# Kernel optimization log

Measured on AMD Instinct MI355X. Metric: run time of the kernel, lower is better.

The kernel has to match this reference:

```python
import jax, jax.numpy as jnp
import numpy as np

N, VQ, VK, C, H = 4, 4096, 4096, 128, 64


def setup_inputs() -> dict:
    key = jax.random.key(0)
    kx, ky, kq, kk, kv = jax.random.split(key, 5)
    # xavier-uniform-ish scale for params
    def xavier(k, shape):
        fan_in, fan_out = shape
        lim = (6.0 / (fan_in + fan_out)) ** 0.5
        return jax.random.uniform(k, shape, jnp.float32, -lim, lim)
    return {
        "x": jax.random.normal(kx, (N, VQ, C), jnp.float32),
        "y": jax.random.normal(ky, (N, VK, C), jnp.float32),
        "Wq": xavier(kq, (C, H)),
        "Wk": xavier(kk, (C, H)),
        "Wv": xavier(kv, (C, C)),
    }


def reference(x, y, Wq, Wk, Wv):
    # x: [n, vq, c], y: [n, vk, c]
    scale = Wq.shape[1] ** (-0.5)
    q = jnp.einsum('nvc,co->nvo', x, Wq)   # [n, vq, h]
    k = jnp.einsum('nvc,co->nvo', y, Wk)   # [n, vk, h]
    v = jnp.einsum('nvc,co->nvo', y, Wv)   # [n, vk, c]
    scores = jnp.einsum('nqc,nkc->nqk', q, k) * scale  # [n, vq, vk]
    attn = jax.nn.softmax(scores, axis=-1)
    return jnp.einsum('nqk,nkc->nqc', attn, v)         # [n, vq, c]
```

## Files before the change

kernel.cpp:

```cpp
#include <hip/hip_runtime.h>

typedef __bf16 bf16x8 __attribute__((ext_vector_type(8)));
typedef __bf16 bf16x4 __attribute__((ext_vector_type(4)));
typedef __bf16 bf16x2 __attribute__((ext_vector_type(2)));
typedef float  f32x4  __attribute__((ext_vector_type(4)));
typedef float  f32x16 __attribute__((ext_vector_type(16)));
typedef int    i32x4  __attribute__((ext_vector_type(4)));

#define MFMA16 __builtin_amdgcn_mfma_f32_16x16x32_bf16
#define MFMA32 __builtin_amdgcn_mfma_f32_32x32x16_bf16

static constexpr int BATCH = 4;
static constexpr int SEQ   = 4096;
static constexpr int CDIM  = 128;
static constexpr int HDIM  = 64;
static constexpr float FIXMAX = 16.0f;

union FB2  { bf16x2 h; int i; };
union I4B8 { i32x4 i; bf16x8 b; };

__device__ inline bf16x8 load8f_cvt(const float* __restrict__ p) {
    f32x4 a = *reinterpret_cast<const f32x4*>(p);
    f32x4 b = *reinterpret_cast<const f32x4*>(p + 4);
    bf16x8 r;
    r[0] = (__bf16)a[0]; r[1] = (__bf16)a[1]; r[2] = (__bf16)a[2]; r[3] = (__bf16)a[3];
    r[4] = (__bf16)b[0]; r[5] = (__bf16)b[1]; r[6] = (__bf16)b[2]; r[7] = (__bf16)b[3];
    return r;
}


__global__ __launch_bounds__(256) void proj_all_kernel(
    const float* __restrict__ x, const float* __restrict__ y,
    const float* __restrict__ Wq, const float* __restrict__ Wk,
    const float* __restrict__ Wv,
    __bf16* __restrict__ Qw, __bf16* __restrict__ Kw, __bf16* __restrict__ Vtw,
    float qscale)
{
    __shared__ __bf16 Wt[64][136];
    __shared__ __bf16 Vtile[64][72];

    const int job = blockIdx.x >> 8;
    const int bx  = blockIdx.x & 255;
    const int t    = threadIdx.x;
    const int lane = t & 63;
    const int w    = t >> 6;
    const int m    = lane & 15;
    const int quad = lane >> 4;

    if (job <= 1) {
        const float* X    = job ? y  : x;
        const float* W    = job ? Wk : Wq;
        __bf16*      outp = job ? Kw : Qw;
        const float scale = job ? 1.0f : qscale;

        #pragma unroll
        for (int pass = 0; pass < 4; ++pass) {
            int flat = pass * 2048 + t * 8;
            int cin  = flat >> 6;
            int h0   = flat & 63;
            bf16x8 v = load8f_cvt(W + flat);
            #pragma unroll
            for (int j = 0; j < 8; ++j) Wt[h0 + j][cin] = v[j];
        }
        __syncthreads();

        const int row0 = bx * 64 + w * 16;
        bf16x8 af[4];
        #pragma unroll
        for (int kc = 0; kc < 4; ++kc)
            af[kc] = load8f_cvt(X + (long)(row0 + m) * 128 + kc * 32 + quad * 8);

        #pragma unroll
        for (int tn = 0; tn < 4; ++tn) {
            f32x4 acc = {0.f, 0.f, 0.f, 0.f};
            #pragma unroll
            for (int kc = 0; kc < 4; ++kc) {
                bf16x8 bfrag = *reinterpret_cast<const bf16x8*>(&Wt[tn * 16 + m][kc * 32 + quad * 8]);
                acc = MFMA16(af[kc], bfrag, acc, 0, 0, 0);
            }
            #pragma unroll
            for (int r = 0; r < 4; ++r) {
                int  kg   = row0 + quad * 4 + r;
                long addr = ((long)(kg >> 5) * 4 + tn) * 512
                          + ((m >> 3) * 32 + (kg & 31)) * 8 + (m & 7);
                outp[addr] = (__bf16)(acc[r] * scale);
            }
        }
    } else {
        const int cob = (job - 2) * 64;
        const int ct0 = (job - 2) * 2;

        #pragma unroll
        for (int pass = 0; pass < 4; ++pass) {
            int flat = pass * 2048 + t * 8;
            int cin  = flat >> 6;
            int co0  = flat & 63;
            bf16x8 v = load8f_cvt(Wv + cin * 128 + cob + co0);
            #pragma unroll
            for (int j = 0; j < 8; ++j) Wt[co0 + j][cin] = v[j];
        }
        __syncthreads();

        const int row0 = bx * 64 + w * 16;
        bf16x8 af[4];
        #pragma unroll
        for (int kc = 0; kc < 4; ++kc)
            af[kc] = load8f_cvt(y + (long)(row0 + m) * 128 + kc * 32 + quad * 8);

        #pragma unroll
        for (int tn = 0; tn < 4; ++tn) {
            f32x4 acc = {0.f, 0.f, 0.f, 0.f};
            #pragma unroll
            for (int kc = 0; kc < 4; ++kc) {
                bf16x8 bfrag = *reinterpret_cast<const bf16x8*>(&Wt[tn * 16 + m][kc * 32 + quad * 8]);
                acc = MFMA16(af[kc], bfrag, acc, 0, 0, 0);
            }
            bf16x4 pk;
            #pragma unroll
            for (int r = 0; r < 4; ++r) pk[r] = (__bf16)acc[r];
            *reinterpret_cast<bf16x4*>(&Vtile[tn * 16 + m][w * 16 + quad * 4]) = pk;
        }
        __syncthreads();

        #pragma unroll
        for (int pp = 0; pp < 2; ++pp) {
            int i       = pp * 256 + t;
            int c_local = i & 31;
            int hh      = (i >> 5) & 1;
            int kc2     = (i >> 6) & 1;
            int ct_l    = (i >> 7) & 1;
            int kt_l    = i >> 8;
            bf16x8 v = *reinterpret_cast<const bf16x8*>(
                &Vtile[ct_l * 32 + c_local][kt_l * 32 + kc2 * 16 + hh * 8]);
            long dst = ((long)(bx * 2 + kt_l) * 8 + (ct0 + ct_l) * 2 + kc2) * 512
                     + (hh * 32 + c_local) * 8;
            *reinterpret_cast<bf16x8*>(Vtw + dst) = v;
        }
    }
}

__device__ __forceinline__ void attn_step(
    const bf16x8 (&kf)[4], const bf16x8 (&vf)[8], const bf16x8 (&qf)[4],
    f32x16 (&o_acc)[4], float& l_a, float& l_b, int h)
{
    f32x16 s;
    #pragma unroll
    for (int i = 0; i < 16; ++i) s[i] = -FIXMAX;
    #pragma unroll
    for (int kc = 0; kc < 4; ++kc)
        s = MFMA32(kf[kc], qf[kc], s, 0, 0, 0);

    int Dw[8];
    #pragma unroll
    for (int r2 = 0; r2 < 8; ++r2) {
        float p0 = __builtin_amdgcn_exp2f(s[2 * r2]);
        float p1 = __builtin_amdgcn_exp2f(s[2 * r2 + 1]);
        l_a += p0; l_b += p1;
        FB2 u; u.h[0] = (__bf16)p0; u.h[1] = (__bf16)p1;
        Dw[r2] = u.i;
    }

    #pragma unroll
    for (int kc2 = 0; kc2 < 2; ++kc2) {
        int a0 = Dw[4 * kc2 + 0], a1 = Dw[4 * kc2 + 1];
        int a2 = Dw[4 * kc2 + 2], a3 = Dw[4 * kc2 + 3];
        int r0 = __shfl_xor(a0, 32, 64);
        int r1 = __shfl_xor(a1, 32, 64);
        int r2 = __shfl_xor(a2, 32, 64);
        int r3 = __shfl_xor(a3, 32, 64);
        I4B8 pb;
        pb.i[0] = h ? r2 : a0;
        pb.i[1] = h ? r3 : a1;
        pb.i[2] = h ? a2 : r0;
        pb.i[3] = h ? a3 : r1;
        #pragma unroll
        for (int ct = 0; ct < 4; ++ct)
            o_acc[ct] = MFMA32(vf[ct * 2 + kc2], pb.b, o_acc[ct], 0, 0, 0);
    }
}

__global__ __launch_bounds__(512, 2) void attn_kernel(
    const __bf16* __restrict__ Qs, const __bf16* __restrict__ Ks,
    const __bf16* __restrict__ Vs, float* __restrict__ out)
{
    __shared__ float mg[2][64][68];

    const int t    = threadIdx.x;
    const int lane = t & 63;
    const int w    = t >> 6;
    const int qh   = w & 1;
    const int g    = w >> 1;
    const int qc   = lane & 31;
    const int h    = lane >> 5;

    const int bx = blockIdx.x;
    const int n  = (bx >> 1) & 3;
    const int qt = (bx >> 3) * 2 + (bx & 1);
    const int q0 = qt * 64 + qh * 32;

    const long QT = (long)n * 128 + (q0 >> 5);
    bf16x8 qf[4];
    #pragma unroll
    for (int kc = 0; kc < 4; ++kc)
        qf[kc] = *reinterpret_cast<const bf16x8*>(Qs + (QT * 4 + kc) * 512 + lane * 8);

    const __bf16* kb = Ks + ((long)n * 128 + g * 32) * 2048 + lane * 8;
    const __bf16* vb = Vs + ((long)n * 128 + g * 32) * 4096 + lane * 8;

    f32x16 o_acc[4];
    #pragma unroll
    for (int ct = 0; ct < 4; ++ct)
        #pragma unroll
        for (int i = 0; i < 16; ++i) o_acc[ct][i] = 0.f;
    float l_a = 0.f, l_b = 0.f;

    bf16x8 kfA[4], vfA[8], kfB[4], vfB[8];

    #pragma unroll
    for (int kc = 0; kc < 4; ++kc)
        kfA[kc] = *reinterpret_cast<const bf16x8*>(kb + kc * 512);
    #pragma unroll
    for (int c = 0; c < 8; ++c)
        vfA[c] = *reinterpret_cast<const bf16x8*>(vb + c * 512);

    for (int kt = 0; kt < 32; kt += 2) {
        {
            const __bf16* kp = kb + (long)(kt + 1) * 2048;
            const __bf16* vp = vb + (long)(kt + 1) * 4096;
            #pragma unroll
            for (int kc = 0; kc < 4; ++kc)
                kfB[kc] = *reinterpret_cast<const bf16x8*>(kp + kc * 512);
            #pragma unroll
            for (int c = 0; c < 8; ++c)
                vfB[c] = *reinterpret_cast<const bf16x8*>(vp + c * 512);
        }
        attn_step(kfA, vfA, qf, o_acc, l_a, l_b, h);

        if (kt < 30) {
            const __bf16* kp = kb + (long)(kt + 2) * 2048;
            const __bf16* vp = vb + (long)(kt + 2) * 4096;
            #pragma unroll
            for (int kc = 0; kc < 4; ++kc)
                kfA[kc] = *reinterpret_cast<const bf16x8*>(kp + kc * 512);
            #pragma unroll
            for (int c = 0; c < 8; ++c)
                vfA[c] = *reinterpret_cast<const bf16x8*>(vp + c * 512);
        }
        attn_step(kfB, vfB, qf, o_acc, l_a, l_b, h);
    }

    float l_run = l_a + l_b;

    for (int gg = 1; gg < 4; ++gg) {
        if (g == gg) {
            float* dst = &mg[qh][lane][0];
            #pragma unroll
            for (int ct = 0; ct < 4; ++ct)
                #pragma unroll
                for (int i = 0; i < 16; ++i)
                    dst[ct * 16 + i] = o_acc[ct][i];
            dst[64] = l_run;
        }
        __syncthreads();
        if (g == 0) {
            const float* src = &mg[qh][lane][0];
            #pragma unroll
            for (int ct = 0; ct < 4; ++ct)
                #pragma unroll
                for (int i = 0; i < 16; ++i)
                    o_acc[ct][i] += src[ct * 16 + i];
            l_run += src[64];
        }
        __syncthreads();
    }

    if (g == 0) {
        l_run += __shfl_xor(l_run, 32, 64);
        const float inv = 1.0f / l_run;
        const long row = (long)n * SEQ + q0 + qc;
        #pragma unroll
        for (int ct = 0; ct < 4; ++ct)
            #pragma unroll
            for (int rg = 0; rg < 4; ++rg) {
                f32x4 o;
                #pragma unroll
                for (int i = 0; i < 4; ++i) o[i] = o_acc[ct][rg * 4 + i] * inv;
                *reinterpret_cast<f32x4*>(out + row * CDIM + ct * 32 + rg * 8 + h * 4) = o;
            }
    }
}

extern "C" void kernel_launch(void* const* d_in, const int* in_sizes, int n_in,
                              void* d_out, int out_size, void* d_ws, size_t ws_size,
                              hipStream_t stream)
{
    const float* x  = (const float*)d_in[0];
    const float* y  = (const float*)d_in[1];
    const float* Wq = (const float*)d_in[2];
    const float* Wk = (const float*)d_in[3];
    const float* Wv = (const float*)d_in[4];
    float* out = (float*)d_out;

    __bf16* Qw  = (__bf16*)d_ws;
    __bf16* Kw  = Qw + (long)BATCH * SEQ * HDIM;
    __bf16* Vtw = Kw + (long)BATCH * SEQ * HDIM;

    const float qscale = 0.125f * 1.4426950408889634f;

    proj_all_kernel<<<dim3(1024), dim3(256), 0, stream>>>(
        x, y, Wq, Wk, Wv, Qw, Kw, Vtw, qscale);

    attn_kernel<<<dim3(256), dim3(512), 0, stream>>>(Qw, Kw, Vtw, out);
}
```

Before: 112.6 us.

## Split each block's keys across eight waves with one query tile and tree reduction

Each block now handles a single 32-row query tile, and all eight waves split the keys (16 tiles each) instead of two query halves times four key groups. The grid doubles to 512 blocks. Launch bounds request four blocks per CU, and the K/V register double buffer shrinks to two K buffers and one V buffer to cut register pressure. The cross-wave merge becomes a three-level tree reduction through shared memory. This aims for more waves in flight and a shorter serial merge, at the cost of reloading Q per block, more reduction traffic, and possible spills under the tighter register budget.

```diff
diff --git a/kernel.cpp b/kernel.cpp
--- a/kernel.cpp
+++ b/kernel.cpp
@@ -179,33 +179,30 @@
     }
 }
 
-__global__ __launch_bounds__(512, 2) void attn_kernel(
+__global__ __launch_bounds__(512, 4) void attn_kernel(
     const __bf16* __restrict__ Qs, const __bf16* __restrict__ Ks,
     const __bf16* __restrict__ Vs, float* __restrict__ out)
 {
-    __shared__ float mg[2][64][68];
+    __shared__ float mbuf[4][64][66];
 
     const int t    = threadIdx.x;
     const int lane = t & 63;
-    const int w    = t >> 6;
-    const int qh   = w & 1;
-    const int g    = w >> 1;
+    const int g    = t >> 6;
     const int qc   = lane & 31;
     const int h    = lane >> 5;
 
-    const int bx = blockIdx.x;
-    const int n  = (bx >> 1) & 3;
-    const int qt = (bx >> 3) * 2 + (bx & 1);
-    const int q0 = qt * 64 + qh * 32;
-
-    const long QT = (long)n * 128 + (q0 >> 5);
+    const int bx  = blockIdx.x;
+    const int n   = bx >> 7;
+    const int qtl = bx & 127;
+
+    const long QT = (long)n * 128 + qtl;
     bf16x8 qf[4];
     #pragma unroll
     for (int kc = 0; kc < 4; ++kc)
         qf[kc] = *reinterpret_cast<const bf16x8*>(Qs + (QT * 4 + kc) * 512 + lane * 8);
 
-    const __bf16* kb = Ks + ((long)n * 128 + g * 32) * 2048 + lane * 8;
-    const __bf16* vb = Vs + ((long)n * 128 + g * 32) * 4096 + lane * 8;
+    const __bf16* kb = Ks + ((long)n * 128 + g * 16) * 2048 + lane * 8;
+    const __bf16* vb = Vs + ((long)n * 128 + g * 16) * 4096 + lane * 8;
 
     f32x16 o_acc[4];
     #pragma unroll
@@ -214,70 +211,99 @@
         for (int i = 0; i < 16; ++i) o_acc[ct][i] = 0.f;
     float l_a = 0.f, l_b = 0.f;
 
-    bf16x8 kfA[4], vfA[8], kfB[4], vfB[8];
+    bf16x8 kf0[4], kf1[4], vf[8];
 
     #pragma unroll
     for (int kc = 0; kc < 4; ++kc)
-        kfA[kc] = *reinterpret_cast<const bf16x8*>(kb + kc * 512);
-    #pragma unroll
-    for (int c = 0; c < 8; ++c)
-        vfA[c] = *reinterpret_cast<const bf16x8*>(vb + c * 512);
-
-    for (int kt = 0; kt < 32; kt += 2) {
+        kf0[kc] = *reinterpret_cast<const bf16x8*>(kb + kc * 512);
+
+    for (int kt = 0; kt < 16; kt += 2) {
         {
+            const __bf16* vp = vb + (long)kt * 4096;
+            #pragma unroll
+            for (int c = 0; c < 8; ++c)
+                vf[c] = *reinterpret_cast<const bf16x8*>(vp + c * 512);
             const __bf16* kp = kb + (long)(kt + 1) * 2048;
+            #pragma unroll
+            for (int kc = 0; kc < 4; ++kc)
+                kf1[kc] = *reinterpret_cast<const bf16x8*>(kp + kc * 512);
+        }
+        attn_step(kf0, vf, qf, o_acc, l_a, l_b, h);
+
+        {
             const __bf16* vp = vb + (long)(kt + 1) * 4096;
             #pragma unroll
-            for (int kc = 0; kc < 4; ++kc)
-                kfB[kc] = *reinterpret_cast<const bf16x8*>(kp + kc * 512);
-            #pragma unroll
             for (int c = 0; c < 8; ++c)
-                vfB[c] = *reinterpret_cast<const bf16x8*>(vp + c * 512);
-        }
-        attn_step(kfA, vfA, qf, o_acc, l_a, l_b, h);
-
-        if (kt < 30) {
-            const __bf16* kp = kb + (long)(kt + 2) * 2048;
-            const __bf16* vp = vb + (long)(kt + 2) * 4096;
-            #pragma unroll
-            for (int kc = 0; kc < 4; ++kc)
-                kfA[kc] = *reinterpret_cast<const bf16x8*>(kp + kc * 512);
-            #pragma unroll
-            for (int c = 0; c < 8; ++c)
-                vfA[c] = *reinterpret_cast<const bf16x8*>(vp + c * 512);
-        }
-        attn_step(kfB, vfB, qf, o_acc, l_a, l_b, h);
+                vf[c] = *reinterpret_cast<const bf16x8*>(vp + c * 512);
+            if (kt < 14) {
+                const __bf16* kp = kb + (long)(kt + 2) * 2048;
+                #pragma unroll
+                for (int kc = 0; kc < 4; ++kc)
+                    kf0[kc] = *reinterpret_cast<const bf16x8*>(kp + kc * 512);
+            }
+        }
+        attn_step(kf1, vf, qf, o_acc, l_a, l_b, h);
     }
 
     float l_run = l_a + l_b;
 
-    for (int gg = 1; gg < 4; ++gg) {
-        if (g == gg) {
-            float* dst = &mg[qh][lane][0];
-            #pragma unroll
-            for (int ct = 0; ct < 4; ++ct)
-                #pragma unroll
-                for (int i = 0; i < 16; ++i)
-                    dst[ct * 16 + i] = o_acc[ct][i];
-            dst[64] = l_run;
-        }
-        __syncthreads();
-        if (g == 0) {
-            const float* src = &mg[qh][lane][0];
-            #pragma unroll
-            for (int ct = 0; ct < 4; ++ct)
-                #pragma unroll
-                for (int i = 0; i < 16; ++i)
-                    o_acc[ct][i] += src[ct * 16 + i];
-            l_run += src[64];
-        }
-        __syncthreads();
-    }
+    if (g >= 4) {
+        float* dst = &mbuf[g - 4][lane][0];
+        #pragma unroll
+        for (int ct = 0; ct < 4; ++ct)
+            #pragma unroll
+            for (int i = 0; i < 16; ++i) dst[ct * 16 + i] = o_acc[ct][i];
+        dst[64] = l_run;
+    }
+    __syncthreads();
+    if (g < 4) {
+        const float* src = &mbuf[g][lane][0];
+        #pragma unroll
+        for (int ct = 0; ct < 4; ++ct)
+            #pragma unroll
+            for (int i = 0; i < 16; ++i) o_acc[ct][i] += src[ct * 16 + i];
+        l_run += src[64];
+    }
+    __syncthreads();
+    if (g == 2 || g == 3) {
+        float* dst = &mbuf[g - 2][lane][0];
+        #pragma unroll
+        for (int ct = 0; ct < 4; ++ct)
+            #pragma unroll
+            for (int i = 0; i < 16; ++i) dst[ct * 16 + i] = o_acc[ct][i];
+        dst[64] = l_run;
+    }
+    __syncthreads();
+    if (g < 2) {
+        const float* src = &mbuf[g][lane][0];
+        #pragma unroll
+        for (int ct = 0; ct < 4; ++ct)
+            #pragma unroll
+            for (int i = 0; i < 16; ++i) o_acc[ct][i] += src[ct * 16 + i];
+        l_run += src[64];
+    }
+    __syncthreads();
+    if (g == 1) {
+        float* dst = &mbuf[0][lane][0];
+        #pragma unroll
+        for (int ct = 0; ct < 4; ++ct)
+            #pragma unroll
+            for (int i = 0; i < 16; ++i) dst[ct * 16 + i] = o_acc[ct][i];
+        dst[64] = l_run;
+    }
+    __syncthreads();
 
     if (g == 0) {
+        const float* src = &mbuf[0][lane][0];
+        #pragma unroll
+        for (int ct = 0; ct < 4; ++ct)
+            #pragma unroll
+            for (int i = 0; i < 16; ++i) o_acc[ct][i] += src[ct * 16 + i];
+        l_run += src[64];
+
         l_run += __shfl_xor(l_run, 32, 64);
         const float inv = 1.0f / l_run;
-        const long row = (long)n * SEQ + q0 + qc;
+        const long row = (long)n * SEQ + qtl * 32 + qc;
         #pragma unroll
         for (int ct = 0; ct < 4; ++ct)
             #pragma unroll
@@ -310,5 +336,5 @@
     proj_all_kernel<<<dim3(1024), dim3(256), 0, stream>>>(
         x, y, Wq, Wk, Wv, Qw, Kw, Vtw, qscale);
 
-    attn_kernel<<<dim3(256), dim3(512), 0, stream>>>(Qw, Kw, Vtw, out);
-}
+    attn_kernel<<<dim3(512), dim3(512), 0, stream>>>(Qw, Kw, Vtw, out);
+}
```

Result: slower. 259.6 us (+130.5%).

## Split attention output channels across warps and double grid size

Applied to the files above, without the earlier changes.

Each block now handles 32 queries rather than 64. The two warp halves split the 128 output channels instead of splitting queries, so every warp recomputes the QK scores for the same 32 queries, and the grid grows to 512 blocks. The register K/V double-buffering is dropped in favour of simple per-iteration loads, and launch bounds are raised to 4 blocks per CU to improve occupancy. The cross-group reduction becomes a two-level tree with fewer barriers. The cost is duplicated QK MFMA and exp work per warp pair, and no explicit prefetch to hide load latency.

```diff
diff --git a/kernel.cpp b/kernel.cpp
--- a/kernel.cpp
+++ b/kernel.cpp
@@ -139,153 +139,137 @@
     }
 }
 
-__device__ __forceinline__ void attn_step(
-    const bf16x8 (&kf)[4], const bf16x8 (&vf)[8], const bf16x8 (&qf)[4],
-    f32x16 (&o_acc)[4], float& l_a, float& l_b, int h)
-{
-    f32x16 s;
-    #pragma unroll
-    for (int i = 0; i < 16; ++i) s[i] = -FIXMAX;
-    #pragma unroll
-    for (int kc = 0; kc < 4; ++kc)
-        s = MFMA32(kf[kc], qf[kc], s, 0, 0, 0);
-
-    int Dw[8];
-    #pragma unroll
-    for (int r2 = 0; r2 < 8; ++r2) {
-        float p0 = __builtin_amdgcn_exp2f(s[2 * r2]);
-        float p1 = __builtin_amdgcn_exp2f(s[2 * r2 + 1]);
-        l_a += p0; l_b += p1;
-        FB2 u; u.h[0] = (__bf16)p0; u.h[1] = (__bf16)p1;
-        Dw[r2] = u.i;
-    }
-
-    #pragma unroll
-    for (int kc2 = 0; kc2 < 2; ++kc2) {
-        int a0 = Dw[4 * kc2 + 0], a1 = Dw[4 * kc2 + 1];
-        int a2 = Dw[4 * kc2 + 2], a3 = Dw[4 * kc2 + 3];
-        int r0 = __shfl_xor(a0, 32, 64);
-        int r1 = __shfl_xor(a1, 32, 64);
-        int r2 = __shfl_xor(a2, 32, 64);
-        int r3 = __shfl_xor(a3, 32, 64);
-        I4B8 pb;
-        pb.i[0] = h ? r2 : a0;
-        pb.i[1] = h ? r3 : a1;
-        pb.i[2] = h ? a2 : r0;
-        pb.i[3] = h ? a3 : r1;
-        #pragma unroll
-        for (int ct = 0; ct < 4; ++ct)
-            o_acc[ct] = MFMA32(vf[ct * 2 + kc2], pb.b, o_acc[ct], 0, 0, 0);
-    }
-}
-
-__global__ __launch_bounds__(512, 2) void attn_kernel(
+__global__ __launch_bounds__(512, 4) void attn_kernel(
     const __bf16* __restrict__ Qs, const __bf16* __restrict__ Ks,
     const __bf16* __restrict__ Vs, float* __restrict__ out)
 {
-    __shared__ float mg[2][64][68];
+    __shared__ float mbuf[2][2][64][33];
 
     const int t    = threadIdx.x;
     const int lane = t & 63;
     const int w    = t >> 6;
-    const int qh   = w & 1;
+    const int ch   = w & 1;
     const int g    = w >> 1;
     const int qc   = lane & 31;
     const int h    = lane >> 5;
 
-    const int bx = blockIdx.x;
-    const int n  = (bx >> 1) & 3;
-    const int qt = (bx >> 3) * 2 + (bx & 1);
-    const int q0 = qt * 64 + qh * 32;
-
-    const long QT = (long)n * 128 + (q0 >> 5);
+    const int bx  = blockIdx.x;
+    const int n   = bx >> 7;
+    const int qtl = bx & 127;
+
+    const long QT = (long)n * 128 + qtl;
     bf16x8 qf[4];
     #pragma unroll
     for (int kc = 0; kc < 4; ++kc)
         qf[kc] = *reinterpret_cast<const bf16x8*>(Qs + (QT * 4 + kc) * 512 + lane * 8);
 
     const __bf16* kb = Ks + ((long)n * 128 + g * 32) * 2048 + lane * 8;
-    const __bf16* vb = Vs + ((long)n * 128 + g * 32) * 4096 + lane * 8;
-
-    f32x16 o_acc[4];
+    const __bf16* vb = Vs + ((long)n * 128 + g * 32) * 4096 + (long)ch * 4 * 512 + lane * 8;
+
+    f32x16 o_acc[2];
     #pragma unroll
-    for (int ct = 0; ct < 4; ++ct)
-        #pragma unroll
-        for (int i = 0; i < 16; ++i) o_acc[ct][i] = 0.f;
+    for (int ctl = 0; ctl < 2; ++ctl)
+        #pragma unroll
+        for (int i = 0; i < 16; ++i) o_acc[ctl][i] = 0.f;
     float l_a = 0.f, l_b = 0.f;
 
-    bf16x8 kfA[4], vfA[8], kfB[4], vfB[8];
-
-    #pragma unroll
-    for (int kc = 0; kc < 4; ++kc)
-        kfA[kc] = *reinterpret_cast<const bf16x8*>(kb + kc * 512);
-    #pragma unroll
-    for (int c = 0; c < 8; ++c)
-        vfA[c] = *reinterpret_cast<const bf16x8*>(vb + c * 512);
-
-    for (int kt = 0; kt < 32; kt += 2) {
-        {
-            const __bf16* kp = kb + (long)(kt + 1) * 2048;
-            const __bf16* vp = vb + (long)(kt + 1) * 4096;
-            #pragma unroll
-            for (int kc = 0; kc < 4; ++kc)
-                kfB[kc] = *reinterpret_cast<const bf16x8*>(kp + kc * 512);
-            #pragma unroll
-            for (int c = 0; c < 8; ++c)
-                vfB[c] = *reinterpret_cast<const bf16x8*>(vp + c * 512);
-        }
-        attn_step(kfA, vfA, qf, o_acc, l_a, l_b, h);
-
-        if (kt < 30) {
-            const __bf16* kp = kb + (long)(kt + 2) * 2048;
-            const __bf16* vp = vb + (long)(kt + 2) * 4096;
-            #pragma unroll
-            for (int kc = 0; kc < 4; ++kc)
-                kfA[kc] = *reinterpret_cast<const bf16x8*>(kp + kc * 512);
-            #pragma unroll
-            for (int c = 0; c < 8; ++c)
-                vfA[c] = *reinterpret_cast<const bf16x8*>(vp + c * 512);
-        }
-        attn_step(kfB, vfB, qf, o_acc, l_a, l_b, h);
+    for (int kt = 0; kt < 32; ++kt) {
+        bf16x8 kf[4], vf[4];
+        const __bf16* kp = kb + (long)kt * 2048;
+        const __bf16* vp = vb + (long)kt * 4096;
+        #pragma unroll
+        for (int kc = 0; kc < 4; ++kc)
+            kf[kc] = *reinterpret_cast<const bf16x8*>(kp + kc * 512);
+        #pragma unroll
+        for (int j = 0; j < 4; ++j)
+            vf[j] = *reinterpret_cast<const bf16x8*>(vp + j * 512);
+
+        f32x16 s;
+        #pragma unroll
+        for (int i = 0; i < 16; ++i) s[i] = -FIXMAX;
+        #pragma unroll
+        for (int kc = 0; kc < 4; ++kc)
+            s = MFMA32(kf[kc], qf[kc], s, 0, 0, 0);
+
+        int Dw[8];
+        #pragma unroll
+        for (int r2 = 0; r2 < 8; ++r2) {
+            float p0 = __builtin_amdgcn_exp2f(s[2 * r2]);
+            float p1 = __builtin_amdgcn_exp2f(s[2 * r2 + 1]);
+            l_a += p0; l_b += p1;
+            FB2 u; u.h[0] = (__bf16)p0; u.h[1] = (__bf16)p1;
+            Dw[r2] = u.i;
+        }
+
+        #pragma unroll
+        for (int kc2 = 0; kc2 < 2; ++kc2) {
+            int a0 = Dw[4 * kc2 + 0], a1 = Dw[4 * kc2 + 1];
+            int a2 = Dw[4 * kc2 + 2], a3 = Dw[4 * kc2 + 3];
+            int r0 = __shfl_xor(a0, 32, 64);
+            int r1 = __shfl_xor(a1, 32, 64);
+            int r2 = __shfl_xor(a2, 32, 64);
+            int r3 = __shfl_xor(a3, 32, 64);
+            I4B8 pb;
+            pb.i[0] = h ? r2 : a0;
+            pb.i[1] = h ? r3 : a1;
+            pb.i[2] = h ? a2 : r0;
+            pb.i[3] = h ? a3 : r1;
+            #pragma unroll
+            for (int ctl = 0; ctl < 2; ++ctl)
+                o_acc[ctl] = MFMA32(vf[ctl * 2 + kc2], pb.b, o_acc[ctl], 0, 0, 0);
+        }
     }
 
     float l_run = l_a + l_b;
 
-    for (int gg = 1; gg < 4; ++gg) {
-        if (g == gg) {
-            float* dst = &mg[qh][lane][0];
-            #pragma unroll
-            for (int ct = 0; ct < 4; ++ct)
-                #pragma unroll
-                for (int i = 0; i < 16; ++i)
-                    dst[ct * 16 + i] = o_acc[ct][i];
-            dst[64] = l_run;
-        }
-        __syncthreads();
-        if (g == 0) {
-            const float* src = &mg[qh][lane][0];
-            #pragma unroll
-            for (int ct = 0; ct < 4; ++ct)
-                #pragma unroll
-                for (int i = 0; i < 16; ++i)
-                    o_acc[ct][i] += src[ct * 16 + i];
-            l_run += src[64];
-        }
-        __syncthreads();
-    }
+    if (g >= 2) {
+        float* dst = &mbuf[ch][g - 2][lane][0];
+        #pragma unroll
+        for (int ctl = 0; ctl < 2; ++ctl)
+            #pragma unroll
+            for (int i = 0; i < 16; ++i) dst[ctl * 16 + i] = o_acc[ctl][i];
+        dst[32] = l_run;
+    }
+    __syncthreads();
+    if (g < 2) {
+        const float* src = &mbuf[ch][g][lane][0];
+        #pragma unroll
+        for (int ctl = 0; ctl < 2; ++ctl)
+            #pragma unroll
+            for (int i = 0; i < 16; ++i) o_acc[ctl][i] += src[ctl * 16 + i];
+        l_run += src[32];
+    }
+    __syncthreads();
+    if (g == 1) {
+        float* dst = &mbuf[ch][0][lane][0];
+        #pragma unroll
+        for (int ctl = 0; ctl < 2; ++ctl)
+            #pragma unroll
+            for (int i = 0; i < 16; ++i) dst[ctl * 16 + i] = o_acc[ctl][i];
+        dst[32] = l_run;
+    }
+    __syncthreads();
 
     if (g == 0) {
+        const float* src = &mbuf[ch][0][lane][0];
+        #pragma unroll
+        for (int ctl = 0; ctl < 2; ++ctl)
+            #pragma unroll
+            for (int i = 0; i < 16; ++i) o_acc[ctl][i] += src[ctl * 16 + i];
+        l_run += src[32];
+
         l_run += __shfl_xor(l_run, 32, 64);
         const float inv = 1.0f / l_run;
-        const long row = (long)n * SEQ + q0 + qc;
-        #pragma unroll
-        for (int ct = 0; ct < 4; ++ct)
+        const long row = (long)n * SEQ + qtl * 32 + qc;
+        #pragma unroll
+        for (int ctl = 0; ctl < 2; ++ctl)
             #pragma unroll
             for (int rg = 0; rg < 4; ++rg) {
                 f32x4 o;
                 #pragma unroll
-                for (int i = 0; i < 4; ++i) o[i] = o_acc[ct][rg * 4 + i] * inv;
-                *reinterpret_cast<f32x4*>(out + row * CDIM + ct * 32 + rg * 8 + h * 4) = o;
+                for (int i = 0; i < 4; ++i) o[i] = o_acc[ctl][rg * 4 + i] * inv;
+                *reinterpret_cast<f32x4*>(
+                    out + row * CDIM + ch * 64 + ctl * 32 + rg * 8 + h * 4) = o;
             }
     }
 }
@@ -310,5 +294,5 @@
     proj_all_kernel<<<dim3(1024), dim3(256), 0, stream>>>(
         x, y, Wq, Wk, Wv, Qw, Kw, Vtw, qscale);
 
-    attn_kernel<<<dim3(256), dim3(512), 0, stream>>>(Qw, Kw, Vtw, out);
-}
+    attn_kernel<<<dim3(512), dim3(512), 0, stream>>>(Qw, Kw, Vtw, out);
+}
```

Result: slower. 123.1 us (+9.3%).

## Restructure attention loop prefetch, tree-reduce split-K partials, remap blocks

Applied to the files above, without the earlier changes.

The main loop now double-buffers only K across iterations and issues the V loads for the current tile after the QK^T MFMAs, which lowers register pressure compared with holding two full K+V buffers. The cross-warp-group reduction becomes a two-level tree (4→2→1) in padded shared memory, replacing the serial three-round accumulation and cutting the number of barriers. The block-to-(batch, q-tile) mapping is changed so consecutive blocks share a batch, which should improve K/V cache locality. The risk is that V load latency is less hidden, since it is fetched within the same iteration it is used.

```diff
diff --git a/kernel.cpp b/kernel.cpp
--- a/kernel.cpp
+++ b/kernel.cpp
@@ -139,66 +139,25 @@
     }
 }
 
-__device__ __forceinline__ void attn_step(
-    const bf16x8 (&kf)[4], const bf16x8 (&vf)[8], const bf16x8 (&qf)[4],
-    f32x16 (&o_acc)[4], float& l_a, float& l_b, int h)
-{
-    f32x16 s;
-    #pragma unroll
-    for (int i = 0; i < 16; ++i) s[i] = -FIXMAX;
-    #pragma unroll
-    for (int kc = 0; kc < 4; ++kc)
-        s = MFMA32(kf[kc], qf[kc], s, 0, 0, 0);
-
-    int Dw[8];
-    #pragma unroll
-    for (int r2 = 0; r2 < 8; ++r2) {
-        float p0 = __builtin_amdgcn_exp2f(s[2 * r2]);
-        float p1 = __builtin_amdgcn_exp2f(s[2 * r2 + 1]);
-        l_a += p0; l_b += p1;
-        FB2 u; u.h[0] = (__bf16)p0; u.h[1] = (__bf16)p1;
-        Dw[r2] = u.i;
-    }
-
-    #pragma unroll
-    for (int kc2 = 0; kc2 < 2; ++kc2) {
-        int a0 = Dw[4 * kc2 + 0], a1 = Dw[4 * kc2 + 1];
-        int a2 = Dw[4 * kc2 + 2], a3 = Dw[4 * kc2 + 3];
-        int r0 = __shfl_xor(a0, 32, 64);
-        int r1 = __shfl_xor(a1, 32, 64);
-        int r2 = __shfl_xor(a2, 32, 64);
-        int r3 = __shfl_xor(a3, 32, 64);
-        I4B8 pb;
-        pb.i[0] = h ? r2 : a0;
-        pb.i[1] = h ? r3 : a1;
-        pb.i[2] = h ? a2 : r0;
-        pb.i[3] = h ? a3 : r1;
-        #pragma unroll
-        for (int ct = 0; ct < 4; ++ct)
-            o_acc[ct] = MFMA32(vf[ct * 2 + kc2], pb.b, o_acc[ct], 0, 0, 0);
-    }
-}
-
 __global__ __launch_bounds__(512, 2) void attn_kernel(
     const __bf16* __restrict__ Qs, const __bf16* __restrict__ Ks,
     const __bf16* __restrict__ Vs, float* __restrict__ out)
 {
-    __shared__ float mg[2][64][68];
+    __shared__ float mbuf[2][2][64][65];
 
     const int t    = threadIdx.x;
     const int lane = t & 63;
     const int w    = t >> 6;
-    const int qh   = w & 1;
+    const int qs   = w & 1;
     const int g    = w >> 1;
     const int qc   = lane & 31;
     const int h    = lane >> 5;
 
-    const int bx = blockIdx.x;
-    const int n  = (bx >> 1) & 3;
-    const int qt = (bx >> 3) * 2 + (bx & 1);
-    const int q0 = qt * 64 + qh * 32;
-
-    const long QT = (long)n * 128 + (q0 >> 5);
+    const int bx  = blockIdx.x;
+    const int n   = bx >> 6;
+    const int qtl = bx & 63;
+
+    const long QT = (long)n * 128 + qtl * 2 + qs;
     bf16x8 qf[4];
     #pragma unroll
     for (int kc = 0; kc < 4; ++kc)
@@ -209,75 +168,112 @@
 
     f32x16 o_acc[4];
     #pragma unroll
-    for (int ct = 0; ct < 4; ++ct)
-        #pragma unroll
-        for (int i = 0; i < 16; ++i) o_acc[ct][i] = 0.f;
+    for (int a = 0; a < 4; ++a)
+        #pragma unroll
+        for (int i = 0; i < 16; ++i) o_acc[a][i] = 0.f;
     float l_a = 0.f, l_b = 0.f;
 
-    bf16x8 kfA[4], vfA[8], kfB[4], vfB[8];
+    bf16x8 kf0[4], kf1[4];
 
     #pragma unroll
     for (int kc = 0; kc < 4; ++kc)
-        kfA[kc] = *reinterpret_cast<const bf16x8*>(kb + kc * 512);
-    #pragma unroll
-    for (int c = 0; c < 8; ++c)
-        vfA[c] = *reinterpret_cast<const bf16x8*>(vb + c * 512);
-
-    for (int kt = 0; kt < 32; kt += 2) {
+        kf0[kc] = *reinterpret_cast<const bf16x8*>(kb + kc * 512);
+
+    for (int kt = 0; kt < 32; ++kt) {
+        const bf16x8 (&kf)[4] = (kt & 1) ? kf1 : kf0;
+        bf16x8 (&kfn)[4]      = (kt & 1) ? kf0 : kf1;
+
+        f32x16 s;
+        #pragma unroll
+        for (int i = 0; i < 16; ++i) s[i] = -FIXMAX;
+        #pragma unroll
+        for (int kc = 0; kc < 4; ++kc)
+            s = MFMA32(kf[kc], qf[kc], s, 0, 0, 0);
+
+        bf16x8 vf[8];
         {
+            const __bf16* vp = vb + (long)kt * 4096;
+            #pragma unroll
+            for (int c = 0; c < 8; ++c)
+                vf[c] = *reinterpret_cast<const bf16x8*>(vp + c * 512);
+        }
+        if (kt < 31) {
             const __bf16* kp = kb + (long)(kt + 1) * 2048;
-            const __bf16* vp = vb + (long)(kt + 1) * 4096;
             #pragma unroll
             for (int kc = 0; kc < 4; ++kc)
-                kfB[kc] = *reinterpret_cast<const bf16x8*>(kp + kc * 512);
-            #pragma unroll
-            for (int c = 0; c < 8; ++c)
-                vfB[c] = *reinterpret_cast<const bf16x8*>(vp + c * 512);
-        }
-        attn_step(kfA, vfA, qf, o_acc, l_a, l_b, h);
-
-        if (kt < 30) {
-            const __bf16* kp = kb + (long)(kt + 2) * 2048;
-            const __bf16* vp = vb + (long)(kt + 2) * 4096;
-            #pragma unroll
-            for (int kc = 0; kc < 4; ++kc)
-                kfA[kc] = *reinterpret_cast<const bf16x8*>(kp + kc * 512);
-            #pragma unroll
-            for (int c = 0; c < 8; ++c)
-                vfA[c] = *reinterpret_cast<const bf16x8*>(vp + c * 512);
-        }
-        attn_step(kfB, vfB, qf, o_acc, l_a, l_b, h);
+                kfn[kc] = *reinterpret_cast<const bf16x8*>(kp + kc * 512);
+        }
+
+        int Dw[8];
+        #pragma unroll
+        for (int r2 = 0; r2 < 8; ++r2) {
+            float p0 = __builtin_amdgcn_exp2f(s[2 * r2]);
+            float p1 = __builtin_amdgcn_exp2f(s[2 * r2 + 1]);
+            l_a += p0; l_b += p1;
+            FB2 u; u.h[0] = (__bf16)p0; u.h[1] = (__bf16)p1;
+            Dw[r2] = u.i;
+        }
+
+        #pragma unroll
+        for (int kc2 = 0; kc2 < 2; ++kc2) {
+            int a0 = Dw[4 * kc2 + 0], a1 = Dw[4 * kc2 + 1];
+            int a2 = Dw[4 * kc2 + 2], a3 = Dw[4 * kc2 + 3];
+            int r0 = __shfl_xor(a0, 32, 64);
+            int r1 = __shfl_xor(a1, 32, 64);
+            int r2 = __shfl_xor(a2, 32, 64);
+            int r3 = __shfl_xor(a3, 32, 64);
+            I4B8 pb;
+            pb.i[0] = h ? r2 : a0;
+            pb.i[1] = h ? r3 : a1;
+            pb.i[2] = h ? a2 : r0;
+            pb.i[3] = h ? a3 : r1;
+            #pragma unroll
+            for (int ct = 0; ct < 4; ++ct)
+                o_acc[ct] = MFMA32(vf[ct * 2 + kc2], pb.b, o_acc[ct], 0, 0, 0);
+        }
     }
 
     float l_run = l_a + l_b;
 
-    for (int gg = 1; gg < 4; ++gg) {
-        if (g == gg) {
-            float* dst = &mg[qh][lane][0];
-            #pragma unroll
-            for (int ct = 0; ct < 4; ++ct)
-                #pragma unroll
-                for (int i = 0; i < 16; ++i)
-                    dst[ct * 16 + i] = o_acc[ct][i];
-            dst[64] = l_run;
-        }
-        __syncthreads();
-        if (g == 0) {
-            const float* src = &mg[qh][lane][0];
-            #pragma unroll
-            for (int ct = 0; ct < 4; ++ct)
-                #pragma unroll
-                for (int i = 0; i < 16; ++i)
-                    o_acc[ct][i] += src[ct * 16 + i];
-            l_run += src[64];
-        }
-        __syncthreads();
-    }
+    if (g >= 2) {
+        float* dst = &mbuf[qs][g - 2][lane][0];
+        #pragma unroll
+        for (int ct = 0; ct < 4; ++ct)
+            #pragma unroll
+            for (int i = 0; i < 16; ++i) dst[ct * 16 + i] = o_acc[ct][i];
+        dst[64] = l_run;
+    }
+    __syncthreads();
+    if (g < 2) {
+        const float* src = &mbuf[qs][g][lane][0];
+        #pragma unroll
+        for (int ct = 0; ct < 4; ++ct)
+            #pragma unroll
+            for (int i = 0; i < 16; ++i) o_acc[ct][i] += src[ct * 16 + i];
+        l_run += src[64];
+    }
+    __syncthreads();
+    if (g == 1) {
+        float* dst = &mbuf[qs][0][lane][0];
+        #pragma unroll
+        for (int ct = 0; ct < 4; ++ct)
+            #pragma unroll
+            for (int i = 0; i < 16; ++i) dst[ct * 16 + i] = o_acc[ct][i];
+        dst[64] = l_run;
+    }
+    __syncthreads();
 
     if (g == 0) {
+        const float* src = &mbuf[qs][0][lane][0];
+        #pragma unroll
+        for (int ct = 0; ct < 4; ++ct)
+            #pragma unroll
+            for (int i = 0; i < 16; ++i) o_acc[ct][i] += src[ct * 16 + i];
+        l_run += src[64];
+
         l_run += __shfl_xor(l_run, 32, 64);
         const float inv = 1.0f / l_run;
-        const long row = (long)n * SEQ + q0 + qc;
+        const long row = (long)n * SEQ + qtl * 64 + qs * 32 + qc;
         #pragma unroll
         for (int ct = 0; ct < 4; ++ct)
             #pragma unroll
@@ -285,7 +281,8 @@
                 f32x4 o;
                 #pragma unroll
                 for (int i = 0; i < 4; ++i) o[i] = o_acc[ct][rg * 4 + i] * inv;
-                *reinterpret_cast<f32x4*>(out + row * CDIM + ct * 32 + rg * 8 + h * 4) = o;
+                *reinterpret_cast<f32x4*>(
+                    out + row * CDIM + ct * 32 + rg * 8 + h * 4) = o;
             }
     }
 }
```

New measurement: 108.2 us. 1.04x faster.
